# Performance work log

Measured on AMD Instinct MI355X. Metric: run time of the kernel, lower is better.

## Reference

```python
import jax, jax.numpy as jnp
import numpy as np

IN_F = 1280
OUT_F = 1280
RANK = 4
NUM_LORAS = 50
LORA_STRIDE = 4
SCALE = 1.0


def setup_inputs() -> dict:
    key = jax.random.key(0)
    k1, k2, k3, k4, k5 = jax.random.split(key, 5)
    x = jax.random.normal(k1, (16, 4096, IN_F), dtype=jnp.float32)
    lora_id = jax.random.randint(k2, (16,), 0, 200)  # raw ids; divided by stride in forward
    W = jax.random.normal(k3, (OUT_F, IN_F), dtype=jnp.float32) * 0.02  # base linear (bias=False)
    # lora_down init: normal(std=1/r); lora_up is zero-init in source but we use small
    # random values so the LoRA path is numerically exercised.
    Wd = jax.random.normal(k4, (NUM_LORAS, RANK, IN_F), dtype=jnp.float32) * (1.0 / RANK)
    Wu = jax.random.normal(k5, (NUM_LORAS, OUT_F, RANK), dtype=jnp.float32) * 0.02
    return {"x": x, "lora_id": lora_id, "W": W, "Wd": Wd, "Wu": Wu}


def reference(x, lora_id, W, Wd, Wu):
    # x: [G, T, D_in]; one chunk per lora_id entry (chunk size 1 along batch).
    idx = lora_id // LORA_STRIDE            # [G] lora index per chunk
    active = lora_id >= 0                   # chunks with negative id skip LoRA
    safe_idx = jnp.where(active, idx, 0)

    base = jnp.einsum('btd,od->bto', x, W)  # dense base linear, shared weight
    # per-chunk gathered low-rank path (dropout is identity in eval mode)
    down = jnp.einsum('btd,brd->btr', x, Wd[safe_idx])   # [G, T, r]
    up = jnp.einsum('btr,bor->bto', down, Wu[safe_idx])  # [G, T, D_out]
    return base + jnp.where(active[:, None, None], up * SCALE, jnp.zeros((), x.dtype))
```

## Files before the change

kernel.cpp:

```cpp
#include <hip/hip_runtime.h>
#include <hip/hip_bf16.h>

typedef __attribute__((ext_vector_type(8))) short short8;
typedef __attribute__((ext_vector_type(4))) short short4v;
typedef __attribute__((ext_vector_type(4))) float f32x4;

#define D_IN 1280
#define D_OUT 1280
#define RANK 4
#define LORA_STRIDE 4
#define BM 128
#define BN 128
#define BK 64

__device__ __forceinline__ short f2bs(float f) {
    __hip_bfloat16 h = __float2bfloat16(f);
    return __builtin_bit_cast(short, h);
}

__device__ __forceinline__ int swz(int row, int k) {
    return row * BK + ((((k >> 3) ^ row) & 7) << 3) + (k & 7);
}

__global__ __launch_bounds__(256, 2)
void lora_fused_gemm(const float* __restrict__ x,
                     const int* __restrict__ lora_id,
                     const float* __restrict__ W,
                     const float* __restrict__ Wd,
                     const float* __restrict__ Wu,
                     float* __restrict__ out,
                     int t_len, int ntiles_n) {
    __shared__ short sA[BM * BK];
    __shared__ short sB[BN * BK];

    const int tid = threadIdx.x;
    const int bx = blockIdx.x;
    const int ntile = bx % ntiles_n;
    const int mtile = bx / ntiles_n;
    const int gm = mtile * BM;
    const int gn = ntile * BN;

    const int chunk = gm / t_len;
    const int lid_raw = lora_id[chunk];
    const bool active = lid_raw >= 0;
    const int idx = active ? (lid_raw / LORA_STRIDE) : 0;
    const float lscale = active ? 1.0f : 0.0f;

    const int arow = tid >> 1;
    const int acol = (tid & 1) * 32;
    const float* xp = x + (long)(gm + arow) * D_IN + acol;

    const int kg = tid & 15;
    const int nr = tid >> 4;
    const float* wp = W + (long)gn * D_IN + kg * 4;
    const float* wdp = Wd + (long)idx * RANK * D_IN + kg * 4;

    f32x4 u[8];
    #pragma unroll
    for (int s = 0; s < 8; ++s) {
        f32x4 t = *reinterpret_cast<const f32x4*>(
            Wu + ((long)idx * D_OUT + gn + nr + 16 * s) * RANK);
        #pragma unroll
        for (int j = 0; j < 4; ++j) u[s][j] = t[j] * lscale;
    }

    const int wave = tid >> 6;
    const int lane = tid & 63;
    const int wm = (wave & 1) * 64;
    const int wn = (wave >> 1) * 64;
    const int quad = lane >> 4;
    const int lr = lane & 15;

    f32x4 acc[4][4];
    #pragma unroll
    for (int a = 0; a < 4; ++a)
        #pragma unroll
        for (int b = 0; b < 4; ++b)
            #pragma unroll
            for (int j = 0; j < 4; ++j) acc[a][b][j] = 0.f;

    for (int k0 = 0; k0 < D_IN; k0 += BK) {
        if (k0) __syncthreads();

        f32x4 xv[8];
        #pragma unroll
        for (int q = 0; q < 8; ++q)
            xv[q] = *reinterpret_cast<const f32x4*>(xp + k0 + q * 4);
        #pragma unroll
        for (int q = 0; q < 4; ++q) {
            short8 v;
            #pragma unroll
            for (int j = 0; j < 4; ++j) {
                v[j]     = f2bs(xv[2 * q][j]);
                v[j + 4] = f2bs(xv[2 * q + 1][j]);
            }
            *reinterpret_cast<short8*>(&sA[swz(arow, acol + q * 8)]) = v;
        }

        f32x4 wd[RANK];
        #pragma unroll
        for (int r = 0; r < RANK; ++r)
            wd[r] = *reinterpret_cast<const f32x4*>(wdp + (long)r * D_IN + k0);
        #pragma unroll
        for (int s = 0; s < 8; ++s) {
            const int n = nr + 16 * s;
            f32x4 wv = *reinterpret_cast<const f32x4*>(wp + (long)n * D_IN + k0);
            short4v e;
            #pragma unroll
            for (int j = 0; j < 4; ++j) {
                float v = wv[j] + u[s][0] * wd[0][j] + u[s][1] * wd[1][j]
                                + u[s][2] * wd[2][j] + u[s][3] * wd[3][j];
                e[j] = f2bs(v);
            }
            *reinterpret_cast<short4v*>(&sB[swz(n, kg * 4)]) = e;
        }

        __syncthreads();

        #pragma unroll
        for (int ks = 0; ks < 2; ++ks) {
            short8 af[4], bfr[4];
            #pragma unroll
            for (int mi = 0; mi < 4; ++mi)
                af[mi] = *reinterpret_cast<const short8*>(
                    &sA[swz(wm + mi * 16 + lr, ks * 32 + quad * 8)]);
            #pragma unroll
            for (int ni = 0; ni < 4; ++ni)
                bfr[ni] = *reinterpret_cast<const short8*>(
                    &sB[swz(wn + ni * 16 + lr, ks * 32 + quad * 8)]);
            #pragma unroll
            for (int mi = 0; mi < 4; ++mi)
                #pragma unroll
                for (int ni = 0; ni < 4; ++ni)
                    acc[mi][ni] = __builtin_amdgcn_mfma_f32_16x16x32_bf16(
                        af[mi], bfr[ni], acc[mi][ni], 0, 0, 0);
        }
    }

    #pragma unroll
    for (int mi = 0; mi < 4; ++mi) {
        #pragma unroll
        for (int ni = 0; ni < 4; ++ni) {
            float* op = out + (long)(gm + wm + mi * 16 + quad * 4) * D_OUT
                            + gn + wn + ni * 16 + lr;
            #pragma unroll
            for (int j = 0; j < 4; ++j) op[(long)j * D_OUT] = acc[mi][ni][j];
        }
    }
}

extern "C" void kernel_launch(void* const* d_in, const int* in_sizes, int n_in,
                              void* d_out, int out_size, void* d_ws, size_t ws_size,
                              hipStream_t stream) {
    const float* x   = (const float*)d_in[0];
    const int* lid   = (const int*)d_in[1];
    const float* W   = (const float*)d_in[2];
    const float* Wd  = (const float*)d_in[3];
    const float* Wu  = (const float*)d_in[4];
    float* out       = (float*)d_out;

    const int M = in_sizes[0] / D_IN;
    const int G = in_sizes[1];
    const int t_len = M / G;
    const int ntiles_n = D_OUT / BN;
    const int nblocks = (M / BM) * ntiles_n;

    lora_fused_gemm<<<nblocks, 256, 0, stream>>>(x, lid, W, Wd, Wu, out, t_len, ntiles_n);
}
```

Measured before the change: 1.180 ms.

## Prefetch next K-tile into registers during MFMA and swizzle block order

Global loads of x, W and Wd for the next K step are issued after the shared-memory barrier and before the MFMA loop, with a sched_barrier, so memory latency overlaps matrix math. Block indices are also remapped across 8 groups (likely for XCD locality on MI355X) so neighboring tiles share cached data. Register pressure rises with 20 extra f32x4 prefetch registers, which may hurt occupancy under launch_bounds(256,2). The remap assumes grid size divisible by 8.

```diff
diff --git a/kernel.cpp b/kernel.cpp
--- a/kernel.cpp
+++ b/kernel.cpp
@@ -34,9 +34,12 @@
     __shared__ short sB[BN * BK];
 
     const int tid = threadIdx.x;
-    const int bx = blockIdx.x;
-    const int ntile = bx % ntiles_n;
-    const int mtile = bx / ntiles_n;
+
+    const int nwg = gridDim.x;
+    const int cpx = nwg >> 3;
+    const int bsw = (blockIdx.x & 7) * cpx + (blockIdx.x >> 3);
+    const int ntile = bsw % ntiles_n;
+    const int mtile = bsw / ntiles_n;
     const int gm = mtile * BM;
     const int gn = ntile * BN;
 
@@ -79,13 +82,20 @@
             #pragma unroll
             for (int j = 0; j < 4; ++j) acc[a][b][j] = 0.f;
 
+    f32x4 xv[8], wd[RANK], wv[8];
+    #pragma unroll
+    for (int q = 0; q < 8; ++q)
+        xv[q] = *reinterpret_cast<const f32x4*>(xp + q * 4);
+    #pragma unroll
+    for (int r = 0; r < RANK; ++r)
+        wd[r] = *reinterpret_cast<const f32x4*>(wdp + (long)r * D_IN);
+    #pragma unroll
+    for (int s = 0; s < 8; ++s)
+        wv[s] = *reinterpret_cast<const f32x4*>(wp + (long)(nr + 16 * s) * D_IN);
+
     for (int k0 = 0; k0 < D_IN; k0 += BK) {
         if (k0) __syncthreads();
 
-        f32x4 xv[8];
-        #pragma unroll
-        for (int q = 0; q < 8; ++q)
-            xv[q] = *reinterpret_cast<const f32x4*>(xp + k0 + q * 4);
         #pragma unroll
         for (int q = 0; q < 4; ++q) {
             short8 v;
@@ -97,25 +107,34 @@
             *reinterpret_cast<short8*>(&sA[swz(arow, acol + q * 8)]) = v;
         }
 
-        f32x4 wd[RANK];
-        #pragma unroll
-        for (int r = 0; r < RANK; ++r)
-            wd[r] = *reinterpret_cast<const f32x4*>(wdp + (long)r * D_IN + k0);
         #pragma unroll
         for (int s = 0; s < 8; ++s) {
             const int n = nr + 16 * s;
-            f32x4 wv = *reinterpret_cast<const f32x4*>(wp + (long)n * D_IN + k0);
             short4v e;
             #pragma unroll
             for (int j = 0; j < 4; ++j) {
-                float v = wv[j] + u[s][0] * wd[0][j] + u[s][1] * wd[1][j]
-                                + u[s][2] * wd[2][j] + u[s][3] * wd[3][j];
+                float v = wv[s][j] + u[s][0] * wd[0][j] + u[s][1] * wd[1][j]
+                                   + u[s][2] * wd[2][j] + u[s][3] * wd[3][j];
                 e[j] = f2bs(v);
             }
             *reinterpret_cast<short4v*>(&sB[swz(n, kg * 4)]) = e;
         }
 
         __syncthreads();
+
+        const int kn = k0 + BK;
+        if (kn < D_IN) {
+            #pragma unroll
+            for (int q = 0; q < 8; ++q)
+                xv[q] = *reinterpret_cast<const f32x4*>(xp + kn + q * 4);
+            #pragma unroll
+            for (int r = 0; r < RANK; ++r)
+                wd[r] = *reinterpret_cast<const f32x4*>(wdp + (long)r * D_IN + kn);
+            #pragma unroll
+            for (int s = 0; s < 8; ++s)
+                wv[s] = *reinterpret_cast<const f32x4*>(wp + (long)(nr + 16 * s) * D_IN + kn);
+        }
+        __builtin_amdgcn_sched_barrier(0);
 
         #pragma unroll
         for (int ks = 0; ks < 2; ++ks) {
```

Result: slower. 1.205 ms (+2.2%).

## Use 256-row tiles with 512 threads and XCD-aware block remapping

Applied to the files above, without the earlier changes.

Adds a kernel variant with 256x128 output tiles computed by 8 waves, so each merged W+LoRA B tile is built once and reused across twice as many rows of x. This halves the per-block recomputation of the bf16 fused weight tile and the reads of W. Block indices are remapped so consecutive tiles land on the same XCD, which should improve L2 reuse. The original 128-row kernel is kept as a fallback when shapes do not divide evenly. The larger tile uses more LDS per block, and the launch bound requests 4 blocks per CU, which may limit registers.

```diff
diff --git a/kernel.cpp b/kernel.cpp
--- a/kernel.cpp
+++ b/kernel.cpp
@@ -9,9 +9,8 @@
 #define D_OUT 1280
 #define RANK 4
 #define LORA_STRIDE 4
-#define BM 128
+#define BK 64
 #define BN 128
-#define BK 64
 
 __device__ __forceinline__ short f2bs(float f) {
     __hip_bfloat16 h = __float2bfloat16(f);
@@ -22,15 +21,147 @@
     return row * BK + ((((k >> 3) ^ row) & 7) << 3) + (k & 7);
 }
 
+__global__ __launch_bounds__(512, 4)
+void lora_fused_gemm_bm256(const float* __restrict__ x,
+                           const int* __restrict__ lora_id,
+                           const float* __restrict__ W,
+                           const float* __restrict__ Wd,
+                           const float* __restrict__ Wu,
+                           float* __restrict__ out,
+                           int t_len, int ntiles_n) {
+    const int BM = 256;
+    __shared__ short sA[256 * BK];
+    __shared__ short sB[BN * BK];
+
+    const int tid = threadIdx.x;
+
+    const int nwg = gridDim.x;
+    const int cpx = nwg >> 3;
+    const int bsw = (blockIdx.x & 7) * cpx + (blockIdx.x >> 3);
+    const int ntile = bsw % ntiles_n;
+    const int mtile = bsw / ntiles_n;
+    const int gm = mtile * BM;
+    const int gn = ntile * BN;
+
+    const int chunk = gm / t_len;
+    const int lid_raw = lora_id[chunk];
+    const bool active = lid_raw >= 0;
+    const int idx = active ? (lid_raw / LORA_STRIDE) : 0;
+    const float lscale = active ? 1.0f : 0.0f;
+
+    const int arow = tid >> 1;
+    const int acol = (tid & 1) * 32;
+    const float* xp = x + (long)(gm + arow) * D_IN + acol;
+
+    const int kg = tid & 15;
+    const int nr = tid >> 4;
+    const float* wp = W + (long)gn * D_IN + kg * 4;
+    const float* wdp = Wd + (long)idx * RANK * D_IN + kg * 4;
+
+    f32x4 u[4];
+    #pragma unroll
+    for (int s = 0; s < 4; ++s) {
+        f32x4 t = *reinterpret_cast<const f32x4*>(
+            Wu + ((long)idx * D_OUT + gn + nr + 32 * s) * RANK);
+        #pragma unroll
+        for (int j = 0; j < 4; ++j) u[s][j] = t[j] * lscale;
+    }
+
+    const int wave = tid >> 6;
+    const int lane = tid & 63;
+    const int wm = (wave & 3) * 64;
+    const int wn = (wave >> 2) * 64;
+    const int quad = lane >> 4;
+    const int lr = lane & 15;
+
+    f32x4 acc[4][4];
+    #pragma unroll
+    for (int a = 0; a < 4; ++a)
+        #pragma unroll
+        for (int b = 0; b < 4; ++b)
+            #pragma unroll
+            for (int j = 0; j < 4; ++j) acc[a][b][j] = 0.f;
+
+    for (int k0 = 0; k0 < D_IN; k0 += BK) {
+        if (k0) __syncthreads();
+
+        f32x4 xv[8];
+        #pragma unroll
+        for (int q = 0; q < 8; ++q)
+            xv[q] = *reinterpret_cast<const f32x4*>(xp + k0 + q * 4);
+        #pragma unroll
+        for (int q = 0; q < 4; ++q) {
+            short8 v;
+            #pragma unroll
+            for (int j = 0; j < 4; ++j) {
+                v[j]     = f2bs(xv[2 * q][j]);
+                v[j + 4] = f2bs(xv[2 * q + 1][j]);
+            }
+            *reinterpret_cast<short8*>(&sA[swz(arow, acol + q * 8)]) = v;
+        }
+
+        f32x4 wd[RANK];
+        #pragma unroll
+        for (int r = 0; r < RANK; ++r)
+            wd[r] = *reinterpret_cast<const f32x4*>(wdp + (long)r * D_IN + k0);
+        #pragma unroll
+        for (int s = 0; s < 4; ++s) {
+            const int n = nr + 32 * s;
+            f32x4 wv = *reinterpret_cast<const f32x4*>(wp + (long)n * D_IN + k0);
+            short4v e;
+            #pragma unroll
+            for (int j = 0; j < 4; ++j) {
+                float v = wv[j] + u[s][0] * wd[0][j] + u[s][1] * wd[1][j]
+                                + u[s][2] * wd[2][j] + u[s][3] * wd[3][j];
+                e[j] = f2bs(v);
+            }
+            *reinterpret_cast<short4v*>(&sB[swz(n, kg * 4)]) = e;
+        }
+
+        __syncthreads();
+
+        #pragma unroll
+        for (int ks = 0; ks < 2; ++ks) {
+            short8 af[4], bfr[4];
+            #pragma unroll
+            for (int mi = 0; mi < 4; ++mi)
+                af[mi] = *reinterpret_cast<const short8*>(
+                    &sA[swz(wm + mi * 16 + lr, ks * 32 + quad * 8)]);
+            #pragma unroll
+            for (int ni = 0; ni < 4; ++ni)
+                bfr[ni] = *reinterpret_cast<const short8*>(
+                    &sB[swz(wn + ni * 16 + lr, ks * 32 + quad * 8)]);
+            #pragma unroll
+            for (int mi = 0; mi < 4; ++mi)
+                #pragma unroll
+                for (int ni = 0; ni < 4; ++ni)
+                    acc[mi][ni] = __builtin_amdgcn_mfma_f32_16x16x32_bf16(
+                        af[mi], bfr[ni], acc[mi][ni], 0, 0, 0);
+        }
+    }
+
+    #pragma unroll
+    for (int mi = 0; mi < 4; ++mi) {
+        #pragma unroll
+        for (int ni = 0; ni < 4; ++ni) {
+            float* op = out + (long)(gm + wm + mi * 16 + quad * 4) * D_OUT
+                            + gn + wn + ni * 16 + lr;
+            #pragma unroll
+            for (int j = 0; j < 4; ++j) op[(long)j * D_OUT] = acc[mi][ni][j];
+        }
+    }
+}
+
 __global__ __launch_bounds__(256, 2)
-void lora_fused_gemm(const float* __restrict__ x,
-                     const int* __restrict__ lora_id,
-                     const float* __restrict__ W,
-                     const float* __restrict__ Wd,
-                     const float* __restrict__ Wu,
-                     float* __restrict__ out,
-                     int t_len, int ntiles_n) {
-    __shared__ short sA[BM * BK];
+void lora_fused_gemm_fb(const float* __restrict__ x,
+                        const int* __restrict__ lora_id,
+                        const float* __restrict__ W,
+                        const float* __restrict__ Wd,
+                        const float* __restrict__ Wu,
+                        float* __restrict__ out,
+                        int t_len, int ntiles_n) {
+    const int BM = 128;
+    __shared__ short sA[128 * BK];
     __shared__ short sB[BN * BK];
 
     const int tid = threadIdx.x;
@@ -163,7 +294,14 @@
     const int G = in_sizes[1];
     const int t_len = M / G;
     const int ntiles_n = D_OUT / BN;
-    const int nblocks = (M / BM) * ntiles_n;
-
-    lora_fused_gemm<<<nblocks, 256, 0, stream>>>(x, lid, W, Wd, Wu, out, t_len, ntiles_n);
-}
+
+    if (M % 256 == 0 && t_len % 256 == 0 && (((M / 256) * ntiles_n) & 7) == 0) {
+        const int nblocks = (M / 256) * ntiles_n;
+        lora_fused_gemm_bm256<<<nblocks, 512, 0, stream>>>(
+            x, lid, W, Wd, Wu, out, t_len, ntiles_n);
+    } else {
+        const int nblocks = (M / 128) * ntiles_n;
+        lora_fused_gemm_fb<<<nblocks, 256, 0, stream>>>(
+            x, lid, W, Wd, Wu, out, t_len, ntiles_n);
+    }
+}
```

New measurement: 1.385 ms. 1.17x slower.
